# Performance work log

Measured on AMD Instinct MI355X. Metric: run time of the kernel, lower is better.

The kernel has to match this reference:

```python
import jax, jax.numpy as jnp
import numpy as np

K = 8
DIM = 128
NUM_BLOCKS = 12


def knn_idx(query, ref, k):
    # query (b,m,3), ref (b,n,3) -> idx (b,m,k) of k nearest refs per query
    d2 = (jnp.sum(query * query, -1)[:, :, None]
          + jnp.sum(ref * ref, -1)[:, None, :]
          - 2.0 * jnp.einsum('bmc,bnc->bmn', query, ref))
    _, idx = jax.lax.top_k(-d2, k)
    return idx


def gather(points, idx):
    # points (b,n,d), idx (b,m,k) -> (b,m,k,d)
    b = points.shape[0]
    return points[jnp.arange(b)[:, None, None], idx]


def feature_net(xyz, w0, w1, w2, k):
    # xyz (b,n,3); self-kNN relative coords then shared MLP, max over neighbors
    idx = knn_idx(xyz, xyz, k)
    grouped = gather(xyz, idx) - xyz[:, :, None, :]      # (b,n,k,3)
    out = jax.nn.relu(jnp.einsum('bnkc,cd->bnkd', grouped, w0))
    out = jax.nn.relu(jnp.einsum('bnkd,de->bnke', out, w1))
    out = jax.nn.relu(jnp.einsum('bnkd,de->bnke', out, w2))
    return jnp.max(out, axis=2)                          # (b,n,dim)


def res_graph_conv_unpool(xyz, points, wc, wn, uc, un, k):
    # xyz (b,n,3), points (b,n,d); wc/wn (12,d,d), uc/un (d,6)
    b, n, _ = xyz.shape
    idx = knn_idx(xyz, xyz, k)
    new_xyz = None
    for i in range(NUM_BLOCKS):
        shortcut = points
        p = jax.nn.relu(points)
        grouped = gather(p, idx)                         # (b,n,k,d)
        center = jnp.einsum('bnd,de->bne', p, wc[i])
        neigh = jnp.einsum('bnkd,de->bne', grouped, wn[i])  # summed over k
        points = (center + neigh) / float(k + 1) + shortcut  # mean over cat(1+k)
        if i == NUM_BLOCKS - 1:
            cx = jnp.einsum('bnd,de->bne', p, uc)        # (b,n,6)
            nx = jnp.einsum('bnkd,de->bne', grouped, un)
            off = (cx + nx) / float(k + 1)               # (b,n,6)
            # torch (b,6,n).view(b,3,2,n): channel j*2+r -> coord j, replica r
            off = off.reshape(b, n, 3, 2)
            off = jnp.transpose(off, (0, 3, 1, 2))       # (b,2,n,3)
            new_xyz = (xyz[:, None, :, :] + off).reshape(b, 2 * n, 3)
    return new_xyz, points


def setup_inputs() -> dict:
    key = jax.random.key(0)
    ks = jax.random.split(key, 12)
    s3 = 1.0 / np.sqrt(3.0)
    sd = 1.0 / np.sqrt(float(DIM))
    return {
        'xyz': jax.random.normal(ks[0], (4, 3, 4096), jnp.float32),
        'fn_w0': jax.random.normal(ks[1], (3, DIM), jnp.float32) * s3,
        'fn_w1': jax.random.normal(ks[2], (DIM, DIM), jnp.float32) * sd,
        'fn_w2': jax.random.normal(ks[3], (DIM, DIM), jnp.float32) * sd,
        'u1_wc': jax.random.normal(ks[4], (NUM_BLOCKS, DIM, DIM), jnp.float32) * sd,
        'u1_wn': jax.random.normal(ks[5], (NUM_BLOCKS, DIM, DIM), jnp.float32) * sd,
        'u1_uc': jax.random.normal(ks[6], (DIM, 6), jnp.float32) * sd,
        'u1_un': jax.random.normal(ks[7], (DIM, 6), jnp.float32) * sd,
        'u2_wc': jax.random.normal(ks[8], (NUM_BLOCKS, DIM, DIM), jnp.float32) * sd,
        'u2_wn': jax.random.normal(ks[9], (NUM_BLOCKS, DIM, DIM), jnp.float32) * sd,
        'u2_uc': jax.random.normal(ks[10], (DIM, 6), jnp.float32) * sd,
        'u2_un': jax.random.normal(ks[11], (DIM, 6), jnp.float32) * sd,
    }


def reference(xyz, fn_w0, fn_w1, fn_w2, u1_wc, u1_wn, u1_uc, u1_un,
              u2_wc, u2_wn, u2_uc, u2_un):
    x = jnp.transpose(xyz, (0, 2, 1))                    # (b,n,3)
    points = feature_net(x, fn_w0, fn_w1, fn_w2, K)      # (b,n,dim)
    new_xyz, points = res_graph_conv_unpool(x, points, u1_wc, u1_wn, u1_uc, u1_un, K)
    # kNN of each new point among the original points, gather + mean
    idx = knn_idx(new_xyz, x, K)                         # (b,2n,k)
    points = jnp.mean(gather(points, idx), axis=2)       # (b,2n,dim)
    new_xyz2, _ = res_graph_conv_unpool(new_xyz, points, u2_wc, u2_wn, u2_uc, u2_un, K)
    return jnp.transpose(new_xyz2, (0, 2, 1))            # (b,3,4n)
```

## Files before the change

kernel.cpp:

```cpp
#include <hip/hip_runtime.h>
#include <hip/hip_bf16.h>

#define NB 12

typedef __attribute__((ext_vector_type(8))) short bf16x8;
typedef __attribute__((ext_vector_type(4))) float f32x4;

#define MFMA16(a, b, c) __builtin_amdgcn_mfma_f32_16x16x32_bf16(a, b, c, 0, 0, 0)

__device__ __forceinline__ unsigned short bf16r(float f) {
  unsigned int u = __float_as_uint(f);
  return (unsigned short)((u + 0x7fffu + ((u >> 16) & 1u)) >> 16);
}

__device__ __forceinline__ float bf2f(unsigned short h) {
  return __uint_as_float(((unsigned int)h) << 16);
}

__device__ __forceinline__ unsigned int fenc(float f) {
  unsigned int u = __float_as_uint(f);
  return (u >> 31) ? ~u : (u | 0x80000000u);
}
__device__ __forceinline__ float fdec(unsigned int e) {
  unsigned int u = (e >> 31) ? (e & 0x7FFFFFFFu) : ~e;
  return __uint_as_float(u);
}

__device__ __forceinline__ float4 relu4(float4 v) {
  v.x = fmaxf(v.x, 0.f); v.y = fmaxf(v.y, 0.f);
  v.z = fmaxf(v.z, 0.f); v.w = fmaxf(v.w, 0.f);
  return v;
}

__device__ __forceinline__ unsigned int pkbf(float x, float y) {
  __hip_bfloat162 h = __float22bfloat162_rn(make_float2(x, y));
  return *reinterpret_cast<unsigned int*>(&h);
}

__device__ __forceinline__ void split8(float4 a, float4 b, bf16x8* ph, bf16x8* pl) {
  unsigned int h01 = pkbf(a.x, a.y), h23 = pkbf(a.z, a.w);
  unsigned int h45 = pkbf(b.x, b.y), h67 = pkbf(b.z, b.w);
  float r0 = a.x - __uint_as_float(h01 << 16);
  float r1 = a.y - __uint_as_float(h01 & 0xFFFF0000u);
  float r2 = a.z - __uint_as_float(h23 << 16);
  float r3 = a.w - __uint_as_float(h23 & 0xFFFF0000u);
  float r4 = b.x - __uint_as_float(h45 << 16);
  float r5 = b.y - __uint_as_float(h45 & 0xFFFF0000u);
  float r6 = b.z - __uint_as_float(h67 << 16);
  float r7 = b.w - __uint_as_float(h67 & 0xFFFF0000u);
  uint4 H = make_uint4(h01, h23, h45, h67);
  uint4 L = make_uint4(pkbf(r0, r1), pkbf(r2, r3), pkbf(r4, r5), pkbf(r6, r7));
  *ph = *reinterpret_cast<bf16x8*>(&H);
  *pl = *reinterpret_cast<bf16x8*>(&L);
}

__global__ __launch_bounds__(256) void k_transpose_in(
    const float* __restrict__ xyz, float* __restrict__ x, int n) {
  int gid = blockIdx.x * 256 + threadIdx.x;
  if (gid >= 4 * n) return;
  int b = gid / n, i = gid % n;
  const float* src = xyz + (size_t)b * 3 * n;
  float* dst = x + (size_t)gid * 3;
  dst[0] = src[i];
  dst[1] = src[n + i];
  dst[2] = src[2 * n + i];
}

__global__ __launch_bounds__(256) void k_wt(
    const float* __restrict__ wc, const float* __restrict__ wn,
    unsigned short* __restrict__ wth, unsigned short* __restrict__ wtl, int total) {
  int tid = blockIdx.x * 256 + threadIdx.x;
  if (tid >= total) return;
  int i = tid >> 15;
  int rem = tid & 32767;
  int e = rem >> 8, d = rem & 255;
  float v = (d < 128) ? wc[i * 16384 + d * 128 + e]
                      : wn[i * 16384 + (d - 128) * 128 + e];
  unsigned short h = bf16r(v);
  wth[tid] = h;
  wtl[tid] = bf16r(v - bf2f(h));
}

__global__ __launch_bounds__(256) void k_frag(
    const float* __restrict__ pts, unsigned short* __restrict__ frag, int n) {
  int gid = blockIdx.x * 256 + threadIdx.x;
  int ntiles = n >> 4;
  if (gid >= 4 * ntiles * 64) return;
  int lane = gid & 63;
  int bt = gid >> 6;
  int b = bt / ntiles, tile = bt % ntiles;
  int rin = lane & 15, kg = lane >> 4;
  const float* p = pts + ((size_t)b * n + tile * 16 + rin) * 3;
  float px = p[0], py = p[1], pz = p[2];
  float rr = px * px + py * py + pz * pz;
  unsigned short h0 = bf16r(px), h1 = bf16r(py), h2 = bf16r(pz);
  unsigned short l0 = bf16r(px - bf2f(h0));
  unsigned short l1 = bf16r(py - bf2f(h1));
  unsigned short l2 = bf16r(pz - bf2f(h2));
  unsigned short rh = bf16r(rr), rl = bf16r(rr - bf2f(rh));
  bf16x8 f = (bf16x8)0;
  if (kg == 0) {
    f[0] = (short)h0; f[1] = (short)h1; f[2] = (short)h2;
    f[3] = (short)l0; f[4] = (short)l1; f[5] = (short)l2;
    f[6] = (short)h0; f[7] = (short)h1;
  } else if (kg == 1) {
    f[0] = (short)h2; f[1] = (short)rh; f[2] = (short)rl;
  }
  *(bf16x8*)(frag + (size_t)gid * 8) = f;
}

#define LCAS(A, B)                                                        \
  {                                                                       \
    bool sw_ = (dist[B] < dist[A]) ||                                     \
               (dist[B] == dist[A] && ind[B] < ind[A]);                   \
    float td_ = sw_ ? dist[A] : dist[B];                                  \
    int ti_ = sw_ ? ind[A] : ind[B];                                      \
    dist[A] = sw_ ? dist[B] : dist[A];                                    \
    ind[A] = sw_ ? ind[B] : ind[A];                                      \
    dist[B] = td_; ind[B] = ti_;                                          \
  }

__global__ __launch_bounds__(256) void k_knn2(
    const float* __restrict__ Q, const float* __restrict__ Rpts,
    const unsigned short* __restrict__ frag,
    int* __restrict__ idx, int M, int N) {
  __shared__ unsigned short chunkbuf[32 * 512];
  __shared__ float smd[4][16][8];
  __shared__ int smi[4][16][8];
  __shared__ unsigned int qgate[32];
  int b = blockIdx.y;
  int t = threadIdx.x;
  int w = t >> 6, lane = t & 63;
  int col = lane & 15, kg = lane >> 4;
  int qg = w & 1, zh = w >> 1;
  int q = blockIdx.x * 32 + qg * 16 + col;
  if (t < 32) qgate[t] = fenc(3.4e38f);
  const float* qp = Q + ((size_t)b * M + q) * 3;
  float qx = qp[0], qy = qp[1], qz = qp[2];
  float qq = qx * qx + qy * qy + qz * qz;
  float m2x = -2.f * qx, m2y = -2.f * qy, m2z = -2.f * qz;
  unsigned short h0 = bf16r(m2x), h1 = bf16r(m2y), h2 = bf16r(m2z);
  unsigned short l0 = bf16r(m2x - bf2f(h0));
  unsigned short l1 = bf16r(m2y - bf2f(h1));
  unsigned short l2 = bf16r(m2z - bf2f(h2));
  bf16x8 bfrag = (bf16x8)0;
  if (kg == 0) {
    bfrag[0] = (short)h0; bfrag[1] = (short)h1; bfrag[2] = (short)h2;
    bfrag[3] = (short)h0; bfrag[4] = (short)h1; bfrag[5] = (short)h2;
    bfrag[6] = (short)l0; bfrag[7] = (short)l1;
  } else if (kg == 1) {
    bfrag[0] = (short)l2;
    bfrag[1] = (short)0x3F80; bfrag[2] = (short)0x3F80;
  }
  float dist[8];
  int ind[8];
#pragma unroll
  for (int j = 0; j < 8; j++) { dist[j] = 3.4e38f; ind[j] = 0; }
  float g8 = 3.4e38f;
  int ntiles = N >> 4;
  int half = ntiles >> 1;
  const unsigned short* fb = frag + (size_t)b * ntiles * 512;
  for (int c = 0; c < half; c += 16) {
    __syncthreads();
    {
      const float4* src = (const float4*)fb;
      float4* dst = (float4*)chunkbuf;
      for (int i = t; i < 1024; i += 256) {
        dst[i] = src[(size_t)c * 64 + i];
        dst[1024 + i] = src[(size_t)(half + c) * 64 + i];
      }
    }
    __syncthreads();
    int lbase = zh * 16;
    int cbase = (zh * half + c) * 16;
    for (int tl = 0; tl < 16; tl++) {
      bf16x8 af = *(const bf16x8*)(&chunkbuf[((lbase + tl) * 64 + lane) * 8]);
      f32x4 z = (f32x4){0.f, 0.f, 0.f, 0.f};
      f32x4 sc = MFMA16(af, bfrag, z);
      float g = fminf(dist[7], g8);
      unsigned int m = 0;
      m |= (sc[0] < g) ? 1u : 0u;
      m |= (sc[1] < g) ? 2u : 0u;
      m |= (sc[2] < g) ? 4u : 0u;
      m |= (sc[3] < g) ? 8u : 0u;
#pragma unroll 1
      for (int it = 0; it < 4; ++it) {
        if (!__any(m != 0u)) break;
        if (m != 0u) {
          int r = (int)__builtin_ctz(m);
          m &= m - 1u;
          float dd = (r & 2) ? ((r & 1) ? sc[3] : sc[2])
                             : ((r & 1) ? sc[1] : sc[0]);
          int ii = cbase + tl * 16 + kg * 4 + r;
#pragma unroll
          for (int j = 0; j < 8; j++) {
            bool sw = dd < dist[j];
            float td = sw ? dist[j] : dd;
            int ti = sw ? ind[j] : ii;
            dist[j] = sw ? dd : dist[j];
            ind[j] = sw ? ii : ind[j];
            dd = td; ii = ti;
          }
        }
      }
    }
    float t1 = fminf(dist[7], __shfl_xor(dist[7], 16, 64));
    float own8 = fminf(t1, __shfl_xor(t1, 32, 64));
    if (kg == 0) atomicMin(&qgate[qg * 16 + col], fenc(own8));
    g8 = fminf(own8, fdec(qgate[qg * 16 + col]));
  }
  {
    const float* Rb2 = Rpts + (size_t)b * N * 3;
    float nd[8];
#pragma unroll
    for (int j = 0; j < 8; j++) {
      int ii = ind[j];
      float rx = Rb2[(size_t)ii * 3 + 0];
      float ry = Rb2[(size_t)ii * 3 + 1];
      float rz = Rb2[(size_t)ii * 3 + 2];
      float rr = rx * rx + ry * ry + rz * rz;
      nd[j] = qq + rr - 2.0f * (qx * rx + qy * ry + qz * rz);
    }
    float sd[8]; int si[8];
#pragma unroll
    for (int j = 0; j < 8; j++) { sd[j] = 3.4e38f; si[j] = 0x7fffffff; }
#pragma unroll
    for (int j = 0; j < 8; j++) {
      float dd = nd[j]; int ii = ind[j];
#pragma unroll
      for (int p = 0; p < 8; p++) {
        bool sw = (dd < sd[p]) || (dd == sd[p] && ii < si[p]);
        float td = sw ? sd[p] : dd;
        int ti = sw ? si[p] : ii;
        sd[p] = sw ? dd : sd[p];
        si[p] = sw ? ii : si[p];
        dd = td; ii = ti;
      }
    }
#pragma unroll
    for (int j = 0; j < 8; j++) { dist[j] = sd[j]; ind[j] = si[j]; }
  }
#pragma unroll
  for (int lev = 0; lev < 2; lev++) {
    int D = 16 << lev;
    float od[8]; int oi[8];
#pragma unroll
    for (int j = 0; j < 8; j++) {
      od[j] = __shfl_xor(dist[j], D, 64);
      oi[j] = __shfl_xor(ind[j], D, 64);
    }
#pragma unroll
    for (int j = 0; j < 8; j++) {
      float bd = od[7 - j]; int bi = oi[7 - j];
      bool take = (bd < dist[j]) || (bd == dist[j] && bi < ind[j]);
      dist[j] = take ? bd : dist[j];
      ind[j] = take ? bi : ind[j];
    }
    LCAS(0, 4) LCAS(1, 5) LCAS(2, 6) LCAS(3, 7)
    LCAS(0, 2) LCAS(1, 3) LCAS(4, 6) LCAS(5, 7)
    LCAS(0, 1) LCAS(2, 3) LCAS(4, 5) LCAS(6, 7)
  }
  if (kg == 0) {
#pragma unroll
    for (int j = 0; j < 8; j++) { smd[w][col][j] = dist[j]; smi[w][col][j] = ind[j]; }
  }
  __syncthreads();
  int tq = t >> 3, jj = t & 7;
  int g = tq >> 4, qcol = tq & 15;
  float d0 = smd[g][qcol][jj];     int i0 = smi[g][qcol][jj];
  float d1 = smd[g + 2][qcol][jj]; int i1 = smi[g + 2][qcol][jj];
  int r0 = jj, r1 = jj;
#pragma unroll
  for (int p = 0; p < 8; p++) {
    float dp = smd[g + 2][qcol][p]; int ip = smi[g + 2][qcol][p];
    r0 += (dp < d0 || (dp == d0 && ip < i0)) ? 1 : 0;
    float dq = smd[g][qcol][p];     int iq = smi[g][qcol][p];
    r1 += (dq < d1 || (dq == d1 && iq < i1)) ? 1 : 0;
  }
  int* o = idx + ((size_t)b * M + blockIdx.x * 32 + tq) * 8;
  if (r0 < 8) o[r0] = i0;
  if (r1 < 8) o[r1] = i1;
}

__global__ __launch_bounds__(256) void k_featnet(
    const float* __restrict__ x, const int* __restrict__ idx,
    const float* __restrict__ w0, const float* __restrict__ w1,
    const float* __restrict__ w2, float* __restrict__ out, int n) {
  __shared__ float X0[64][128];
  __shared__ float X1[64][128];
  int b = blockIdx.y;
  int q0 = blockIdx.x * 8;
  int t = threadIdx.x;
  {
    int row = t >> 2, seg = t & 3;
    int qi = row >> 3, j = row & 7;
    size_t qb = (size_t)b * n + (q0 + qi);
    const float* qp = x + qb * 3;
    int nb = idx[qb * 8 + j];
    const float* pp = x + ((size_t)b * n + nb) * 3;
    float r0 = pp[0] - qp[0], r1 = pp[1] - qp[1], r2 = pp[2] - qp[2];
    int c0 = seg * 32;
#pragma unroll
    for (int u = 0; u < 8; u++) {
      int cc = c0 + u * 4;
      float4 a = *(const float4*)(w0 + cc);
      float4 bb = *(const float4*)(w0 + 128 + cc);
      float4 cv = *(const float4*)(w0 + 256 + cc);
      float4 h;
      h.x = fmaxf(fmaf(r0, a.x, fmaf(r1, bb.x, r2 * cv.x)), 0.f);
      h.y = fmaxf(fmaf(r0, a.y, fmaf(r1, bb.y, r2 * cv.y)), 0.f);
      h.z = fmaxf(fmaf(r0, a.z, fmaf(r1, bb.z, r2 * cv.z)), 0.f);
      h.w = fmaxf(fmaf(r0, a.w, fmaf(r1, bb.w, r2 * cv.w)), 0.f);
      *(float4*)(&X0[row][cc]) = h;
    }
  }
  __syncthreads();
  int rg = t >> 5, cg = t & 31;
  int r0r = rg * 8, c0 = cg * 4;
  float acc[8][4];
#pragma unroll
  for (int i = 0; i < 8; i++)
#pragma unroll
    for (int c = 0; c < 4; c++) acc[i][c] = 0.f;
  for (int e = 0; e < 128; e++) {
    float4 w = *(const float4*)(w1 + e * 128 + c0);
#pragma unroll
    for (int i = 0; i < 8; i++) {
      float xi = X0[r0r + i][e];
      acc[i][0] = fmaf(xi, w.x, acc[i][0]);
      acc[i][1] = fmaf(xi, w.y, acc[i][1]);
      acc[i][2] = fmaf(xi, w.z, acc[i][2]);
      acc[i][3] = fmaf(xi, w.w, acc[i][3]);
    }
  }
#pragma unroll
  for (int i = 0; i < 8; i++) {
    float4 h;
    h.x = fmaxf(acc[i][0], 0.f); h.y = fmaxf(acc[i][1], 0.f);
    h.z = fmaxf(acc[i][2], 0.f); h.w = fmaxf(acc[i][3], 0.f);
    *(float4*)(&X1[r0r + i][c0]) = h;
  }
  __syncthreads();
#pragma unroll
  for (int i = 0; i < 8; i++)
#pragma unroll
    for (int c = 0; c < 4; c++) acc[i][c] = 0.f;
  for (int e = 0; e < 128; e++) {
    float4 w = *(const float4*)(w2 + e * 128 + c0);
#pragma unroll
    for (int i = 0; i < 8; i++) {
      float xi = X1[r0r + i][e];
      acc[i][0] = fmaf(xi, w.x, acc[i][0]);
      acc[i][1] = fmaf(xi, w.y, acc[i][1]);
      acc[i][2] = fmaf(xi, w.z, acc[i][2]);
      acc[i][3] = fmaf(xi, w.w, acc[i][3]);
    }
  }
  float4 m; m.x = 0.f; m.y = 0.f; m.z = 0.f; m.w = 0.f;
#pragma unroll
  for (int i = 0; i < 8; i++) {
    m.x = fmaxf(m.x, acc[i][0]); m.y = fmaxf(m.y, acc[i][1]);
    m.z = fmaxf(m.z, acc[i][2]); m.w = fmaxf(m.w, acc[i][3]);
  }
  *(float4*)(out + ((size_t)b * n + q0 + rg) * 128 + c0) = m;
}

__global__ __launch_bounds__(256) void k_conv(
    const float* __restrict__ Pin, float* __restrict__ Pout,
    const int* __restrict__ idx, const unsigned short* __restrict__ wth,
    const unsigned short* __restrict__ wtl, int n) {
  __shared__ unsigned short Xh[32 * 256];
  __shared__ unsigned short Xl[32 * 256];
  int b = blockIdx.y, t = threadIdx.x;
  int rblk = blockIdx.x * 32;
  {
    int row = t >> 3, seg = t & 7;
    size_t rb = (size_t)b * n + rblk + row;
    const float4* src = (const float4*)(Pin + rb * 128 + seg * 16);
    float4 cv[4];
#pragma unroll
    for (int u = 0; u < 4; u++) cv[u] = relu4(src[u]);
    const int* ip = idx + rb * 8;
    float4 ns[4];
#pragma unroll
    for (int u = 0; u < 4; u++) ns[u] = make_float4(0.f, 0.f, 0.f, 0.f);
#pragma unroll
    for (int j = 0; j < 8; j++) {
      const float4* s2 = (const float4*)(Pin + ((size_t)b * n + ip[j]) * 128 + seg * 16);
#pragma unroll
      for (int u = 0; u < 4; u++) {
        float4 v = relu4(s2[u]);
        ns[u].x += v.x; ns[u].y += v.y; ns[u].z += v.z; ns[u].w += v.w;
      }
    }
#pragma unroll
    for (int u = 0; u < 2; u++) {
      int lc = seg * 2 + u;
      int ph = (row * 256 + ((lc ^ (row & 7)) * 8));
      split8(cv[2 * u], cv[2 * u + 1], (bf16x8*)&Xh[ph], (bf16x8*)&Xl[ph]);
      int lc2 = 16 + seg * 2 + u;
      int ph2 = (row * 256 + ((lc2 ^ (row & 7)) * 8));
      split8(ns[2 * u], ns[2 * u + 1], (bf16x8*)&Xh[ph2], (bf16x8*)&Xl[ph2]);
    }
  }
  __syncthreads();
  int w = t >> 6, lane = t & 63;
  int lo = lane & 15, hi = lane >> 4;
  f32x4 acc[2][2];
#pragma unroll
  for (int mt = 0; mt < 2; mt++)
#pragma unroll
    for (int nt = 0; nt < 2; nt++) acc[mt][nt] = (f32x4){0.f, 0.f, 0.f, 0.f};
  const unsigned short* wbh = wth + ((size_t)(w * 32 + lo) * 256 + hi * 8);
  const unsigned short* wbl = wtl + ((size_t)(w * 32 + lo) * 256 + hi * 8);
#pragma unroll
  for (int kk = 0; kk < 8; kk++) {
    bf16x8 ah[2], al[2];
#pragma unroll
    for (int mt = 0; mt < 2; mt++) {
      int row = mt * 16 + lo;
      int off = row * 256 + (((4 * kk + hi) ^ (row & 7)) * 8);
      ah[mt] = *(const bf16x8*)(&Xh[off]);
      al[mt] = *(const bf16x8*)(&Xl[off]);
    }
    bf16x8 bh0 = *(const bf16x8*)(wbh + kk * 32);
    bf16x8 bh1 = *(const bf16x8*)(wbh + 4096 + kk * 32);
    bf16x8 bl0 = *(const bf16x8*)(wbl + kk * 32);
    bf16x8 bl1 = *(const bf16x8*)(wbl + 4096 + kk * 32);
#pragma unroll
    for (int mt = 0; mt < 2; mt++) {
      acc[mt][0] = MFMA16(ah[mt], bh0, acc[mt][0]);
      acc[mt][0] = MFMA16(ah[mt], bl0, acc[mt][0]);
      acc[mt][0] = MFMA16(al[mt], bh0, acc[mt][0]);
      acc[mt][1] = MFMA16(ah[mt], bh1, acc[mt][1]);
      acc[mt][1] = MFMA16(ah[mt], bl1, acc[mt][1]);
      acc[mt][1] = MFMA16(al[mt], bh1, acc[mt][1]);
    }
  }
  const float inv9 = 1.0f / 9.0f;
#pragma unroll
  for (int mt = 0; mt < 2; mt++)
#pragma unroll
    for (int nt = 0; nt < 2; nt++) {
      int col = w * 32 + nt * 16 + lo;
#pragma unroll
      for (int r = 0; r < 4; r++) {
        int row = rblk + mt * 16 + hi * 4 + r;
        size_t off = ((size_t)b * n + row) * 128 + col;
        Pout[off] = fmaf(acc[mt][nt][r], inv9, Pin[off]);
      }
    }
}

__global__ __launch_bounds__(256) void k_unpool(
    const float* __restrict__ Pin, const int* __restrict__ idx,
    const float* __restrict__ xin,
    const float* __restrict__ uc, const float* __restrict__ un,
    float* __restrict__ out, int n, int transposed) {
  int b = blockIdx.y;
  int wv = threadIdx.x >> 6, lane = threadIdx.x & 63;
  int i = blockIdx.x * 4 + wv;
  if (i >= n) return;
  size_t rb = (size_t)b * n + i;
  const float* p0 = Pin + rb * 128;
  float pd0 = fmaxf(p0[lane], 0.f), pd1 = fmaxf(p0[lane + 64], 0.f);
  const int* ip = idx + rb * 8;
  float ns0 = 0.f, ns1 = 0.f;
#pragma unroll
  for (int j = 0; j < 8; j++) {
    const float* pj = Pin + ((size_t)b * n + ip[j]) * 128;
    ns0 += fmaxf(pj[lane], 0.f);
    ns1 += fmaxf(pj[lane + 64], 0.f);
  }
  float acc[6];
#pragma unroll
  for (int o = 0; o < 6; o++)
    acc[o] = pd0 * uc[lane * 6 + o] + pd1 * uc[(lane + 64) * 6 + o] +
             ns0 * un[lane * 6 + o] + ns1 * un[(lane + 64) * 6 + o];
#pragma unroll
  for (int s = 32; s > 0; s >>= 1) {
#pragma unroll
    for (int o = 0; o < 6; o++) acc[o] += __shfl_xor(acc[o], s, 64);
  }
  if (lane < 6) {
    int j = lane >> 1, r = lane & 1;
    float v = xin[rb * 3 + j] + acc[lane] * (1.0f / 9.0f);
    if (transposed)
      out[(size_t)b * 6 * n + (size_t)j * 2 * n + (size_t)r * n + i] = v;
    else
      out[((size_t)b * 2 * n + (size_t)r * n + i) * 3 + j] = v;
  }
}

__global__ __launch_bounds__(256) void k_meangather(
    const float* __restrict__ Pin, const int* __restrict__ idx,
    float* __restrict__ Pout, int M, int nsrc) {
  int gid = blockIdx.x * 256 + threadIdx.x;
  int row = gid >> 6, lane = gid & 63;
  if (row >= 4 * M) return;
  int b = row / M;
  const int* ip = idx + (size_t)row * 8;
  float s0 = 0.f, s1 = 0.f;
#pragma unroll
  for (int j = 0; j < 8; j++) {
    const float* p = Pin + ((size_t)b * nsrc + ip[j]) * 128;
    s0 += p[lane];
    s1 += p[lane + 64];
  }
  Pout[(size_t)row * 128 + lane] = s0 * 0.125f;
  Pout[(size_t)row * 128 + lane + 64] = s1 * 0.125f;
}

extern "C" void kernel_launch(void* const* d_in, const int* in_sizes, int n_in,
                              void* d_out, int out_size, void* d_ws, size_t ws_size,
                              hipStream_t stream) {
  const float* xyz = (const float*)d_in[0];
  const float* fw0 = (const float*)d_in[1];
  const float* fw1 = (const float*)d_in[2];
  const float* fw2 = (const float*)d_in[3];
  const float* u1wc = (const float*)d_in[4];
  const float* u1wn = (const float*)d_in[5];
  const float* u1uc = (const float*)d_in[6];
  const float* u1un = (const float*)d_in[7];
  const float* u2wc = (const float*)d_in[8];
  const float* u2wn = (const float*)d_in[9];
  const float* u2uc = (const float*)d_in[10];
  const float* u2un = (const float*)d_in[11];
  float* out = (float*)d_out;

  const int n1 = 4096, n2 = 8192, B = 4;
  float* ws = (float*)d_ws;
  float* x = ws;
  float* nxz = x + (size_t)B * n1 * 3;
  int* idx1 = (int*)(nxz + (size_t)B * n2 * 3);
  int* idx2g = idx1 + (size_t)B * n1 * 8;
  int* idx2s = idx2g + (size_t)B * n2 * 8;
  float* A = (float*)(idx2s + (size_t)B * n2 * 8);
  float* Bb = A + (size_t)B * n2 * 128;
  unsigned short* wt1h = (unsigned short*)(Bb + (size_t)B * n2 * 128);
  unsigned short* wt1l = wt1h + (size_t)NB * 128 * 256;
  unsigned short* wt2h = wt1l + (size_t)NB * 128 * 256;
  unsigned short* wt2l = wt2h + (size_t)NB * 128 * 256;
  unsigned short* fragx = wt2l + (size_t)NB * 128 * 256;
  unsigned short* fragn = fragx + (size_t)B * (n1 / 16) * 512;

  const int wtot = NB * 128 * 256;
  k_wt<<<dim3((wtot + 255) / 256), 256, 0, stream>>>(u1wc, u1wn, wt1h, wt1l, wtot);
  k_wt<<<dim3((wtot + 255) / 256), 256, 0, stream>>>(u2wc, u2wn, wt2h, wt2l, wtot);

  k_transpose_in<<<dim3((B * n1 + 255) / 256), 256, 0, stream>>>(xyz, x, n1);
  k_frag<<<dim3(B * (n1 / 16) * 64 / 256), 256, 0, stream>>>(x, fragx, n1);
  k_knn2<<<dim3(n1 / 32, B), 256, 0, stream>>>(x, x, fragx, idx1, n1, n1);
  k_featnet<<<dim3(n1 / 8, B), 256, 0, stream>>>(x, idx1, fw0, fw1, fw2, A, n1);
  for (int i = 0; i < NB; i++) {
    const float* pin = (i & 1) ? Bb : A;
    float* pout = (i & 1) ? A : Bb;
    k_conv<<<dim3(n1 / 32, B), 256, 0, stream>>>(
        pin, pout, idx1, wt1h + (size_t)i * 128 * 256, wt1l + (size_t)i * 128 * 256, n1);
  }
  k_unpool<<<dim3(n1 / 4, B), 256, 0, stream>>>(Bb, idx1, x, u1uc, u1un, nxz, n1, 0);
  k_frag<<<dim3(B * (n2 / 16) * 64 / 256), 256, 0, stream>>>(nxz, fragn, n2);
  k_knn2<<<dim3(n2 / 32, B), 256, 0, stream>>>(nxz, x, fragx, idx2g, n2, n1);
  k_meangather<<<dim3((B * n2 * 64 + 255) / 256), 256, 0, stream>>>(A, idx2g, Bb, n2, n1);
  k_knn2<<<dim3(n2 / 32, B), 256, 0, stream>>>(nxz, nxz, fragn, idx2s, n2, n2);
  for (int i = 0; i < NB; i++) {
    const float* pin = (i & 1) ? A : Bb;
    float* pout = (i & 1) ? Bb : A;
    k_conv<<<dim3(n2 / 32, B), 256, 0, stream>>>(
        pin, pout, idx2s, wt2h + (size_t)i * 128 * 256, wt2l + (size_t)i * 128 * 256, n2);
  }
  k_unpool<<<dim3(n2 / 4, B), 256, 0, stream>>>(A, idx2s, nxz, u2uc, u2un, out, n2, 1);
}
```

Baseline: 1.210 ms.

## Move feature-net MLP to bf16x3 MFMA and remap conv grid across batches

Rewrites the feature-net kernel so its two 128x128 layers run on MFMA with split hi/lo bf16 operands (three products per tile), using swizzled LDS staging and a warp-shuffle max over neighbors, in place of scalar FP32 FMA loops. Weights are pre-split into bf16 hi/lo by a new small kernel. Separately, the conv launch is flattened to a 1D grid whose block index interleaves batches, spreading neighboring blocks across batches to change cache/XCD locality. The split-bf16 scheme approximates FP32 precision and adds extra LDS traffic.

```diff
diff --git a/kernel.cpp b/kernel.cpp
--- a/kernel.cpp
+++ b/kernel.cpp
@@ -79,6 +79,17 @@
   unsigned short h = bf16r(v);
   wth[tid] = h;
   wtl[tid] = bf16r(v - bf2f(h));
+}
+
+__global__ __launch_bounds__(256) void k_wtf(
+    const float* __restrict__ w, unsigned short* __restrict__ wh,
+    unsigned short* __restrict__ wl) {
+  int tid = blockIdx.x * 256 + threadIdx.x;
+  int e = tid >> 7, d = tid & 127;
+  float v = w[d * 128 + e];
+  unsigned short h = bf16r(v);
+  wh[tid] = h;
+  wl[tid] = bf16r(v - bf2f(h));
 }
 
 __global__ __launch_bounds__(256) void k_frag(
@@ -282,87 +293,149 @@
   if (r1 < 8) o[r1] = i1;
 }
 
-__global__ __launch_bounds__(256) void k_featnet(
+__global__ __launch_bounds__(256) void k_featnet2(
     const float* __restrict__ x, const int* __restrict__ idx,
-    const float* __restrict__ w0, const float* __restrict__ w1,
-    const float* __restrict__ w2, float* __restrict__ out, int n) {
-  __shared__ float X0[64][128];
-  __shared__ float X1[64][128];
-  int b = blockIdx.y;
+    const float* __restrict__ w0,
+    const unsigned short* __restrict__ w1h, const unsigned short* __restrict__ w1l,
+    const unsigned short* __restrict__ w2h, const unsigned short* __restrict__ w2l,
+    float* __restrict__ out, int n) {
+  __shared__ unsigned short Xh[64 * 128];
+  __shared__ unsigned short Xl[64 * 128];
+  __shared__ float F[64 * 128];
+  int b = blockIdx.y, t = threadIdx.x;
   int q0 = blockIdx.x * 8;
-  int t = threadIdx.x;
   {
     int row = t >> 2, seg = t & 3;
     int qi = row >> 3, j = row & 7;
-    size_t qb = (size_t)b * n + (q0 + qi);
+    size_t qb = (size_t)b * n + q0 + qi;
     const float* qp = x + qb * 3;
     int nb = idx[qb * 8 + j];
     const float* pp = x + ((size_t)b * n + nb) * 3;
     float r0 = pp[0] - qp[0], r1 = pp[1] - qp[1], r2 = pp[2] - qp[2];
-    int c0 = seg * 32;
-#pragma unroll
-    for (int u = 0; u < 8; u++) {
-      int cc = c0 + u * 4;
-      float4 a = *(const float4*)(w0 + cc);
-      float4 bb = *(const float4*)(w0 + 128 + cc);
-      float4 cv = *(const float4*)(w0 + 256 + cc);
-      float4 h;
-      h.x = fmaxf(fmaf(r0, a.x, fmaf(r1, bb.x, r2 * cv.x)), 0.f);
-      h.y = fmaxf(fmaf(r0, a.y, fmaf(r1, bb.y, r2 * cv.y)), 0.f);
-      h.z = fmaxf(fmaf(r0, a.z, fmaf(r1, bb.z, r2 * cv.z)), 0.f);
-      h.w = fmaxf(fmaf(r0, a.w, fmaf(r1, bb.w, r2 * cv.w)), 0.f);
-      *(float4*)(&X0[row][cc]) = h;
+#pragma unroll
+    for (int u = 0; u < 4; u++) {
+      int cc = seg * 32 + u * 8;
+      float h[8];
+#pragma unroll
+      for (int v = 0; v < 8; v++) {
+        int c = cc + v;
+        h[v] = fmaxf(fmaf(r0, w0[c], fmaf(r1, w0[128 + c], r2 * w0[256 + c])), 0.f);
+      }
+      float4 a = make_float4(h[0], h[1], h[2], h[3]);
+      float4 bb = make_float4(h[4], h[5], h[6], h[7]);
+      int lc = seg * 4 + u;
+      int ph = row * 128 + ((lc ^ (row & 7)) * 8);
+      split8(a, bb, (bf16x8*)&Xh[ph], (bf16x8*)&Xl[ph]);
     }
   }
   __syncthreads();
-  int rg = t >> 5, cg = t & 31;
-  int r0r = rg * 8, c0 = cg * 4;
-  float acc[8][4];
-#pragma unroll
-  for (int i = 0; i < 8; i++)
-#pragma unroll
-    for (int c = 0; c < 4; c++) acc[i][c] = 0.f;
-  for (int e = 0; e < 128; e++) {
-    float4 w = *(const float4*)(w1 + e * 128 + c0);
-#pragma unroll
-    for (int i = 0; i < 8; i++) {
-      float xi = X0[r0r + i][e];
-      acc[i][0] = fmaf(xi, w.x, acc[i][0]);
-      acc[i][1] = fmaf(xi, w.y, acc[i][1]);
-      acc[i][2] = fmaf(xi, w.z, acc[i][2]);
-      acc[i][3] = fmaf(xi, w.w, acc[i][3]);
-    }
-  }
-#pragma unroll
-  for (int i = 0; i < 8; i++) {
-    float4 h;
-    h.x = fmaxf(acc[i][0], 0.f); h.y = fmaxf(acc[i][1], 0.f);
-    h.z = fmaxf(acc[i][2], 0.f); h.w = fmaxf(acc[i][3], 0.f);
-    *(float4*)(&X1[r0r + i][c0]) = h;
-  }
+  int w = t >> 6, lane = t & 63;
+  int lo = lane & 15, hi = lane >> 4;
+  f32x4 acc[4][2];
+#pragma unroll
+  for (int mt = 0; mt < 4; mt++)
+#pragma unroll
+    for (int nt = 0; nt < 2; nt++) acc[mt][nt] = (f32x4){0.f, 0.f, 0.f, 0.f};
+  {
+    const unsigned short* wbh = w1h + ((size_t)(w * 32 + lo) * 128 + hi * 8);
+    const unsigned short* wbl = w1l + ((size_t)(w * 32 + lo) * 128 + hi * 8);
+#pragma unroll
+    for (int kk = 0; kk < 4; kk++) {
+      bf16x8 ah[4], al[4];
+#pragma unroll
+      for (int mt = 0; mt < 4; mt++) {
+        int row = mt * 16 + lo;
+        int off = row * 128 + (((4 * kk + hi) ^ (row & 7)) * 8);
+        ah[mt] = *(const bf16x8*)(&Xh[off]);
+        al[mt] = *(const bf16x8*)(&Xl[off]);
+      }
+      bf16x8 bh0 = *(const bf16x8*)(wbh + kk * 32);
+      bf16x8 bh1 = *(const bf16x8*)(wbh + 16 * 128 + kk * 32);
+      bf16x8 bl0 = *(const bf16x8*)(wbl + kk * 32);
+      bf16x8 bl1 = *(const bf16x8*)(wbl + 16 * 128 + kk * 32);
+#pragma unroll
+      for (int mt = 0; mt < 4; mt++) {
+        acc[mt][0] = MFMA16(ah[mt], bh0, acc[mt][0]);
+        acc[mt][0] = MFMA16(ah[mt], bl0, acc[mt][0]);
+        acc[mt][0] = MFMA16(al[mt], bh0, acc[mt][0]);
+        acc[mt][1] = MFMA16(ah[mt], bh1, acc[mt][1]);
+        acc[mt][1] = MFMA16(ah[mt], bl1, acc[mt][1]);
+        acc[mt][1] = MFMA16(al[mt], bh1, acc[mt][1]);
+      }
+    }
+  }
+#pragma unroll
+  for (int mt = 0; mt < 4; mt++)
+#pragma unroll
+    for (int nt = 0; nt < 2; nt++) {
+      int colc = w * 32 + nt * 16 + lo;
+      int chunk = colc >> 2, cr = colc & 3;
+#pragma unroll
+      for (int r = 0; r < 4; r++) {
+        int row = mt * 16 + hi * 4 + r;
+        F[row * 128 + ((chunk ^ ((row & 7) << 2)) << 2) + cr] = acc[mt][nt][r];
+      }
+    }
   __syncthreads();
-#pragma unroll
-  for (int i = 0; i < 8; i++)
-#pragma unroll
-    for (int c = 0; c < 4; c++) acc[i][c] = 0.f;
-  for (int e = 0; e < 128; e++) {
-    float4 w = *(const float4*)(w2 + e * 128 + c0);
-#pragma unroll
-    for (int i = 0; i < 8; i++) {
-      float xi = X1[r0r + i][e];
-      acc[i][0] = fmaf(xi, w.x, acc[i][0]);
-      acc[i][1] = fmaf(xi, w.y, acc[i][1]);
-      acc[i][2] = fmaf(xi, w.z, acc[i][2]);
-      acc[i][3] = fmaf(xi, w.w, acc[i][3]);
-    }
-  }
-  float4 m; m.x = 0.f; m.y = 0.f; m.z = 0.f; m.w = 0.f;
-#pragma unroll
-  for (int i = 0; i < 8; i++) {
-    m.x = fmaxf(m.x, acc[i][0]); m.y = fmaxf(m.y, acc[i][1]);
-    m.z = fmaxf(m.z, acc[i][2]); m.w = fmaxf(m.w, acc[i][3]);
-  }
-  *(float4*)(out + ((size_t)b * n + q0 + rg) * 128 + c0) = m;
+  {
+    int row = t >> 2, seg = t & 3;
+#pragma unroll
+    for (int u = 0; u < 4; u++) {
+      int cc = (seg * 32 + u * 8) >> 2;
+      int pc = cc ^ ((row & 7) << 2);
+      float4 a = *(const float4*)(&F[row * 128 + pc * 4]);
+      float4 bb = *(const float4*)(&F[row * 128 + (pc + 1) * 4]);
+      a = relu4(a); bb = relu4(bb);
+      int lc = seg * 4 + u;
+      int ph = row * 128 + ((lc ^ (row & 7)) * 8);
+      split8(a, bb, (bf16x8*)&Xh[ph], (bf16x8*)&Xl[ph]);
+    }
+  }
+  __syncthreads();
+#pragma unroll
+  for (int mt = 0; mt < 4; mt++)
+#pragma unroll
+    for (int nt = 0; nt < 2; nt++) acc[mt][nt] = (f32x4){0.f, 0.f, 0.f, 0.f};
+  {
+    const unsigned short* wbh = w2h + ((size_t)(w * 32 + lo) * 128 + hi * 8);
+    const unsigned short* wbl = w2l + ((size_t)(w * 32 + lo) * 128 + hi * 8);
+#pragma unroll
+    for (int kk = 0; kk < 4; kk++) {
+      bf16x8 ah[4], al[4];
+#pragma unroll
+      for (int mt = 0; mt < 4; mt++) {
+        int row = mt * 16 + lo;
+        int off = row * 128 + (((4 * kk + hi) ^ (row & 7)) * 8);
+        ah[mt] = *(const bf16x8*)(&Xh[off]);
+        al[mt] = *(const bf16x8*)(&Xl[off]);
+      }
+      bf16x8 bh0 = *(const bf16x8*)(wbh + kk * 32);
+      bf16x8 bh1 = *(const bf16x8*)(wbh + 16 * 128 + kk * 32);
+      bf16x8 bl0 = *(const bf16x8*)(wbl + kk * 32);
+      bf16x8 bl1 = *(const bf16x8*)(wbl + 16 * 128 + kk * 32);
+#pragma unroll
+      for (int mt = 0; mt < 4; mt++) {
+        acc[mt][0] = MFMA16(ah[mt], bh0, acc[mt][0]);
+        acc[mt][0] = MFMA16(ah[mt], bl0, acc[mt][0]);
+        acc[mt][0] = MFMA16(al[mt], bh0, acc[mt][0]);
+        acc[mt][1] = MFMA16(ah[mt], bh1, acc[mt][1]);
+        acc[mt][1] = MFMA16(ah[mt], bl1, acc[mt][1]);
+        acc[mt][1] = MFMA16(al[mt], bh1, acc[mt][1]);
+      }
+    }
+  }
+#pragma unroll
+  for (int mt = 0; mt < 4; mt++)
+#pragma unroll
+    for (int nt = 0; nt < 2; nt++) {
+      float m = fmaxf(fmaxf(acc[mt][nt][0], acc[mt][nt][1]),
+                      fmaxf(acc[mt][nt][2], acc[mt][nt][3]));
+      float o = fmaxf(m, __shfl_xor(m, 16, 64));
+      if ((hi & 1) == 0) {
+        int q = q0 + mt * 2 + (hi >> 1);
+        out[((size_t)b * n + q) * 128 + w * 32 + nt * 16 + lo] = fmaxf(o, 0.f);
+      }
+    }
 }
 
 __global__ __launch_bounds__(256) void k_conv(
@@ -371,8 +444,11 @@
     const unsigned short* __restrict__ wtl, int n) {
   __shared__ unsigned short Xh[32 * 256];
   __shared__ unsigned short Xl[32 * 256];
-  int b = blockIdx.y, t = threadIdx.x;
-  int rblk = blockIdx.x * 32;
+  int t = threadIdx.x;
+  int fid = blockIdx.x;
+  int x8 = fid & 7;
+  int b = x8 >> 1;
+  int rblk = ((fid >> 3) * 2 + (x8 & 1)) * 32;
   {
     int row = t >> 3, seg = t & 7;
     size_t rb = (size_t)b * n + rblk + row;
@@ -543,19 +619,25 @@
   unsigned short* wt2l = wt2h + (size_t)NB * 128 * 256;
   unsigned short* fragx = wt2l + (size_t)NB * 128 * 256;
   unsigned short* fragn = fragx + (size_t)B * (n1 / 16) * 512;
+  unsigned short* f1h = fragn + (size_t)B * (n2 / 16) * 512;
+  unsigned short* f1l = f1h + 16384;
+  unsigned short* f2h = f1l + 16384;
+  unsigned short* f2l = f2h + 16384;
 
   const int wtot = NB * 128 * 256;
   k_wt<<<dim3((wtot + 255) / 256), 256, 0, stream>>>(u1wc, u1wn, wt1h, wt1l, wtot);
   k_wt<<<dim3((wtot + 255) / 256), 256, 0, stream>>>(u2wc, u2wn, wt2h, wt2l, wtot);
+  k_wtf<<<dim3(64), 256, 0, stream>>>(fw1, f1h, f1l);
+  k_wtf<<<dim3(64), 256, 0, stream>>>(fw2, f2h, f2l);
 
   k_transpose_in<<<dim3((B * n1 + 255) / 256), 256, 0, stream>>>(xyz, x, n1);
   k_frag<<<dim3(B * (n1 / 16) * 64 / 256), 256, 0, stream>>>(x, fragx, n1);
   k_knn2<<<dim3(n1 / 32, B), 256, 0, stream>>>(x, x, fragx, idx1, n1, n1);
-  k_featnet<<<dim3(n1 / 8, B), 256, 0, stream>>>(x, idx1, fw0, fw1, fw2, A, n1);
+  k_featnet2<<<dim3(n1 / 8, B), 256, 0, stream>>>(x, idx1, fw0, f1h, f1l, f2h, f2l, A, n1);
   for (int i = 0; i < NB; i++) {
     const float* pin = (i & 1) ? Bb : A;
     float* pout = (i & 1) ? A : Bb;
-    k_conv<<<dim3(n1 / 32, B), 256, 0, stream>>>(
+    k_conv<<<dim3((n1 / 32) * B), 256, 0, stream>>>(
         pin, pout, idx1, wt1h + (size_t)i * 128 * 256, wt1l + (size_t)i * 128 * 256, n1);
   }
   k_unpool<<<dim3(n1 / 4, B), 256, 0, stream>>>(Bb, idx1, x, u1uc, u1un, nxz, n1, 0);
@@ -566,7 +648,7 @@
   for (int i = 0; i < NB; i++) {
     const float* pin = (i & 1) ? A : Bb;
     float* pout = (i & 1) ? Bb : A;
-    k_conv<<<dim3(n2 / 32, B), 256, 0, stream>>>(
+    k_conv<<<dim3((n2 / 32) * B), 256, 0, stream>>>(
         pin, pout, idx2s, wt2h + (size_t)i * 128 * 256, wt2l + (size_t)i * 128 * 256, n2);
   }
   k_unpool<<<dim3(n2 / 4, B), 256, 0, stream>>>(A, idx2s, nxz, u2uc, u2un, out, n2, 1);
```

Result: faster. 1.086 ms (-10.2%).
